# Kernel optimization log

Hardware: AMD Instinct MI355X
Metric: run time of the kernel (lower is better)

The kernel has to match this reference:

```python
import jax, jax.numpy as jnp
import numpy as np

# Dims: B=2, S=2048, D=1024 hidden, E=8 experts, F=2752 ffn (SwiGLU), top-1 gate,
# capacity_factor=1.0 -> capacity C = (B*S)//E = 512. Residual-MoE (moe_use_residual=True).

def setup_inputs() -> dict:
    key = jax.random.key(0)
    ks = jax.random.split(key, 10)
    B, S, D, E, F = 2, 2048, 1024, 8, 2752
    sc = 0.02
    return {
        "hidden_states": jax.random.normal(ks[0], (B, S, D), jnp.float32),
        "wg":  jax.random.normal(ks[1], (D, E), jnp.float32) * sc,   # gate
        "w1":  jax.random.normal(ks[2], (E, D, F), jnp.float32) * sc,  # expert SwiGLU
        "w3":  jax.random.normal(ks[3], (E, D, F), jnp.float32) * sc,
        "w2":  jax.random.normal(ks[4], (E, F, D), jnp.float32) * sc,
        "rw1": jax.random.normal(ks[5], (D, F), jnp.float32) * sc,    # residual MLP (SwiGLU, no bias)
        "rw3": jax.random.normal(ks[6], (D, F), jnp.float32) * sc,
        "rw2": jax.random.normal(ks[7], (F, D), jnp.float32) * sc,
        "cw":  jax.random.normal(ks[8], (D, 2), jnp.float32) * sc,    # coefficient Linear(D, 2)
        "cb":  jnp.zeros((2,), jnp.float32),
    }


def _moe_forward(x, wg, w1, w3, w2):
    """GShard/DeepSpeed-style top-1 gated MoE with capacity + token dropping.
    x: [T, D] flattened tokens. Returns (out [T,D], l_aux scalar, exp_counts [E])."""
    T, D = x.shape
    E = wg.shape[1]
    C = max(4, T // E)  # capacity_factor = 1.0, min_capacity = 4

    logits = x @ wg                                  # [T, E]
    gates = jax.nn.softmax(logits, axis=-1)
    idx = jnp.argmax(gates, axis=-1)                 # top-1 expert per token
    mask1 = jax.nn.one_hot(idx, E, dtype=gates.dtype)  # [T, E]
    exp_counts = jnp.sum(mask1, axis=0).astype(jnp.int32)

    # load-balancing aux loss (DeepSpeed top1gating)
    me = jnp.mean(gates, axis=0)
    ce = jnp.mean(mask1, axis=0)
    l_aux = jnp.sum(me * ce) * E

    # position of each token within its expert's buffer; drop overflow
    locations = jnp.cumsum(mask1, axis=0) - 1.0      # [T, E]
    mask1 = mask1 * (locations < C)
    loc_s = jnp.sum(locations * mask1, axis=1).astype(jnp.int32)  # [T]
    gates1 = jnp.sum(gates * mask1, axis=1)          # [T] gate weight (0 if dropped)

    loc_oh = jax.nn.one_hot(loc_s, C, dtype=gates.dtype)          # [T, C]
    combine = gates1[:, None, None] * mask1[:, :, None] * loc_oh[:, None, :]  # [T, E, C]
    dispatch = (combine > 0).astype(x.dtype)

    xe = jnp.einsum("tec,td->ecd", dispatch, x)      # dispatch to [E, C, D]
    h = jax.nn.silu(jnp.einsum("ecd,edf->ecf", xe, w1)) * jnp.einsum("ecd,edf->ecf", xe, w3)
    ye = jnp.einsum("ecf,efd->ecd", h, w2)           # expert SwiGLU FFN
    out = jnp.einsum("tec,ecd->td", combine, ye)     # weighted combine back to tokens
    return out, l_aux, exp_counts


def reference(hidden_states, wg, w1, w3, w2, rw1, rw3, rw2, cw, cb):
    B, S, D = hidden_states.shape
    x = hidden_states.reshape(-1, D)
    moe_out, l_aux, exp_counts = _moe_forward(x, wg, w1, w3, w2)
    moe_out = moe_out.reshape(B, S, D)

    # residual SwiGLU MLP + softmax-gated combine (Residual-MoE)
    mlp = (jax.nn.silu(hidden_states @ rw1) * (hidden_states @ rw3)) @ rw2
    coef = jax.nn.softmax(hidden_states @ cw + cb, axis=-1)  # [B, S, 2]
    output = moe_out * coef[..., 0:1] + mlp * coef[..., 1:2]
    return output, l_aux, exp_counts
```

## Files before the change

kernel.cpp:

```cpp
#include <hip/hip_runtime.h>
#include <hip/hip_bf16.h>
#include <stdint.h>

#define T_TOK 4096
#define DD 1024
#define EE 8
#define CC 512
#define FF 2752
#define FP 2816

typedef __attribute__((ext_vector_type(8))) short bf16x8;
typedef __attribute__((ext_vector_type(4))) float f32x4;
typedef __attribute__((ext_vector_type(4))) unsigned short us4;
typedef __attribute__((ext_vector_type(8))) unsigned short us8;

__device__ __forceinline__ float bf2f(unsigned short u) {
  union { float f; unsigned int i; } v; v.i = ((unsigned int)u) << 16; return v.f;
}
__device__ __forceinline__ unsigned short f2bf(float f) {
  union { float f; unsigned int i; } v; v.f = f;
  unsigned int r = v.i + 0x7fffu + ((v.i >> 16) & 1u);
  return (unsigned short)(r >> 16);
}

#define GLDS16(g, l) __builtin_amdgcn_global_load_lds( \
    (const __attribute__((address_space(1))) void*)(g), \
    (__attribute__((address_space(3))) void*)(l), 16, 0, 0)

#define STG_CHUNK(l) (((l & 3) ^ ((l >> 3) & 3)) * 8)
#define RD_OFF(fr, fq) ((fr) * 32 + (((fq) ^ (((fr) >> 1) & 3)) * 8))

#define BAR() do { asm volatile("" ::: "memory"); __builtin_amdgcn_s_barrier(); \
                   asm volatile("" ::: "memory"); } while (0)

template<int RT>
__global__ __launch_bounds__(256)
void transpose_k(const float* __restrict__ in, const float* __restrict__ in2,
                 unsigned short* __restrict__ out, unsigned short* __restrict__ out2,
                 int R, int C, long inStride, long outStride) {
  __shared__ unsigned short sm[RT * 64];
  int b = blockIdx.z;
  if (b < EE) { in += (long)b * inStride; out += (long)b * outStride; }
  else { in = in2; out = out2; }
  int cb = blockIdx.x * 64, rb = blockIdx.y * RT;
  int t = threadIdx.x;
  int rr = t >> 4, c4 = (t & 15) * 4;
#pragma unroll
  for (int i = 0; i < RT / 16; ++i) {
    int r = rr + i * 16;
    float4 v = *(const float4*)(in + (long)(rb + r) * C + cb + c4);
    us4 o; o.x = f2bf(v.x); o.y = f2bf(v.y); o.z = f2bf(v.z); o.w = f2bf(v.w);
    *(us4*)&sm[r * 64 + (c4 ^ (((r >> 3) & 7) << 3))] = o;
  }
  __syncthreads();
#pragma unroll
  for (int j = 0; j < (64 * (RT / 8)) / 256; ++j) {
    int idx = t + j * 256;
    int g, c;
    if (RT == 128) { g = idx & 15; c = idx >> 4; }
    else           { g = idx & 7;  c = idx >> 3; }
    int r8 = g * 8;
    us8 o;
#pragma unroll
    for (int k = 0; k < 8; ++k) {
      int r = r8 + k;
      o[k] = sm[r * 64 + (c ^ (((r >> 3) & 7) << 3))];
    }
    *(us8*)(out + (long)(cb + c) * R + rb + r8) = o;
  }
}

__global__ void zero_me_k(float* me) { if (threadIdx.x < EE) me[threadIdx.x] = 0.0f; }

__global__ void gate_k(const float* __restrict__ x, const float* __restrict__ wg,
                       const float* __restrict__ cw, const float* __restrict__ cbv,
                       int* __restrict__ idx, float* __restrict__ gatev,
                       float* __restrict__ coef, float* __restrict__ me_sum) {
  int tid = threadIdx.x, lane = tid & 63, wv = tid >> 6;
  int t = blockIdx.x * 4 + wv;
  const float* xr = x + (long)t * DD;
  float acc[EE] = {0,0,0,0,0,0,0,0};
  float c0 = 0.0f, c1 = 0.0f;
  for (int d = lane; d < DD; d += 64) {
    float xv = xr[d];
#pragma unroll
    for (int e = 0; e < EE; ++e) acc[e] += xv * wg[d * EE + e];
    c0 += xv * cw[d * 2 + 0];
    c1 += xv * cw[d * 2 + 1];
  }
#pragma unroll
  for (int o = 32; o > 0; o >>= 1) {
#pragma unroll
    for (int e = 0; e < EE; ++e) acc[e] += __shfl_xor(acc[e], o);
    c0 += __shfl_xor(c0, o);
    c1 += __shfl_xor(c1, o);
  }
  __shared__ float sme[EE];
  if (tid < EE) sme[tid] = 0.0f;
  __syncthreads();
  if (lane == 0) {
    float m = acc[0]; int am = 0;
#pragma unroll
    for (int e = 1; e < EE; ++e) if (acc[e] > m) { m = acc[e]; am = e; }
    float g[EE]; float s = 0.0f;
#pragma unroll
    for (int e = 0; e < EE; ++e) { g[e] = __expf(acc[e] - m); s += g[e]; }
    float inv = 1.0f / s;
    idx[t] = am;
    gatev[t] = g[am] * inv;
#pragma unroll
    for (int e = 0; e < EE; ++e) atomicAdd(&sme[e], g[e] * inv);
    float l0 = c0 + cbv[0], l1 = c1 + cbv[1];
    float mm = fmaxf(l0, l1);
    float e0 = __expf(l0 - mm), e1 = __expf(l1 - mm);
    float is = 1.0f / (e0 + e1);
    coef[t * 2 + 0] = e0 * is;
    coef[t * 2 + 1] = e1 * is;
  }
  __syncthreads();
  if (tid < EE) atomicAdd(&me_sum[tid], sme[tid]);
}

__global__ void scan_k(const int* __restrict__ idx, const float* __restrict__ me_sum,
                       int* __restrict__ slot, int* __restrict__ tok,
                       float* __restrict__ out_tail) {
  __shared__ int sidx[T_TOK];
  __shared__ int counts[EE];
  int tid = threadIdx.x;
  for (int i = tid; i < T_TOK; i += 512) sidx[i] = idx[i];
  __syncthreads();
  int e = tid >> 6, lane = tid & 63;
  int base = 0;
  for (int it = 0; it < T_TOK / 64; ++it) {
    int t = it * 64 + lane;
    bool f = (sidx[t] == e);
    unsigned long long m = __ballot(f);
    if (f) {
      int loc = base + __popcll(m & ((1ull << lane) - 1ull));
      slot[t] = (loc < CC) ? loc : -1;
      if (loc < CC) tok[e * CC + loc] = t;
    }
    base += __popcll(m);
  }
  if (lane == 0) counts[e] = base;
  __syncthreads();
  int filled = min(counts[e], CC);
  for (int c = filled + lane; c < CC; c += 64) tok[e * CC + c] = -1;
  if (tid == 0) {
    float la = 0.0f;
    for (int i = 0; i < EE; ++i) la += me_sum[i] * (float)counts[i];
    la *= (float)EE / ((float)T_TOK * (float)T_TOK);
    out_tail[0] = la;
    for (int i = 0; i < EE; ++i) out_tail[1 + i] = (float)counts[i];
  }
}

__global__ void gather_k(const float* __restrict__ x, const int* __restrict__ tok,
                         unsigned short* __restrict__ xb, unsigned short* __restrict__ xe) {
  int r = blockIdx.x, tid = threadIdx.x;
  int d = tid * 4;
  if (r < T_TOK) {
    float4 v = *(const float4*)(x + (long)r * DD + d);
    us4 o; o.x = f2bf(v.x); o.y = f2bf(v.y); o.z = f2bf(v.z); o.w = f2bf(v.w);
    *(us4*)(xb + (long)r * DD + d) = o;
  } else {
    int s = r - T_TOK;
    int t = tok[s];
    us4 o = {0, 0, 0, 0};
    if (t >= 0) {
      float4 v = *(const float4*)(x + (long)t * DD + d);
      o.x = f2bf(v.x); o.y = f2bf(v.y); o.z = f2bf(v.z); o.w = f2bf(v.w);
    }
    *(us4*)(xe + (long)s * DD + d) = o;
  }
}

__global__ __launch_bounds__(512, 2)
void gemm1_k(const unsigned short* __restrict__ xcat,
             const unsigned short* __restrict__ w1t, const unsigned short* __restrict__ w3t,
             const unsigned short* __restrict__ rw1t, const unsigned short* __restrict__ rw3t,
             unsigned short* __restrict__ Hcat) {
  int lin = blockIdx.x;
  int work = (lin & 7) * 88 + (lin >> 3);
  int mtile, ntile;
  if (work < 352) {
    int e = work / 44, r = work - e * 44;
    ntile = r >> 1;
    mtile = e * 2 + (r & 1);
  } else {
    int q = work - 352;
    ntile = q >> 4;
    mtile = 16 + (q & 15);
  }
  const unsigned short* A = xcat + (size_t)mtile * 256 * DD;
  const unsigned short *B1, *B3;
  if (mtile < 16) { int e = mtile >> 1; B1 = w1t + (size_t)e * FP * DD; B3 = w3t + (size_t)e * FP * DD; }
  else { B1 = rw1t; B3 = rw3t; }
  unsigned short* H = Hcat + (size_t)mtile * 256 * FF;
  int n0 = ntile * 128;

  __shared__ __align__(16) unsigned short lds[65536];
  char* L = (char*)lds;

  int tid = threadIdx.x, l = tid & 63, w = tid >> 6;
  int wm = w >> 1, wn = w & 1;
  int fr = l & 15, fq = l >> 4;
  int srow = l >> 2, soff = STG_CHUNK(l);
  int rdo = RD_OFF(fr, fq);

  const unsigned short* gA0 = A + (size_t)(w * 16 + srow) * DD + soff;
  const unsigned short* gA1 = A + (size_t)((8 + w) * 16 + srow) * DD + soff;
  const unsigned short* gB1 = B1 + (size_t)(n0 + w * 16 + srow) * DD + soff;
  const unsigned short* gB3 = B3 + (size_t)(n0 + w * 16 + srow) * DD + soff;

#define STG_A(ss, kk, ks) do {                                                    \
    GLDS16(gA0 + (kk) + (ks) * 32, L + (ss) * 32768 + (ks) * 16384 + w * 1024);   \
    GLDS16(gA1 + (kk) + (ks) * 32, L + (ss) * 32768 + (ks) * 16384 + (8 + w) * 1024); } while (0)
#define STG_B(ss, kk, ks) do {                                                    \
    GLDS16(gB1 + (kk) + (ks) * 32, L + 65536 + (ss) * 16384 + (ks) * 8192 + w * 1024); \
    GLDS16(gB3 + (kk) + (ks) * 32, L + 98304 + (ss) * 16384 + (ks) * 8192 + w * 1024); } while (0)

  f32x4 acc1[4][4] = {};
  f32x4 acc3[4][4] = {};
  bf16x8 af[4], b1f[4], b3f[4];

  const int NT = DD / 64;
  STG_A(0, 0, 0); STG_B(0, 0, 0); STG_A(0, 0, 1); STG_B(0, 0, 1);

  for (int t = 0; t < NT; ++t) {
    int s = t & 1, ns = s ^ 1;
    int kk1 = ((t + 1 < NT) ? t + 1 : 0) * 64;

    STG_A(ns, kk1, 0);
    asm volatile("s_waitcnt vmcnt(6)" ::: "memory");
#pragma unroll
    for (int mi = 0; mi < 4; ++mi)
      af[mi] = *(const bf16x8*)(lds + s * 16384 + (wm * 4 + mi) * 512 + rdo);
#pragma unroll
    for (int ni = 0; ni < 4; ++ni)
      b1f[ni] = *(const bf16x8*)(lds + 32768 + s * 8192 + (wn * 4 + ni) * 512 + rdo);
    BAR();
    __builtin_amdgcn_s_setprio(1);
#pragma unroll
    for (int mi = 0; mi < 4; ++mi)
#pragma unroll
      for (int ni = 0; ni < 4; ++ni)
        acc1[mi][ni] = __builtin_amdgcn_mfma_f32_16x16x32_bf16(af[mi], b1f[ni], acc1[mi][ni], 0, 0, 0);
    __builtin_amdgcn_s_setprio(0);
    BAR();

#pragma unroll
    for (int ni = 0; ni < 4; ++ni)
      b3f[ni] = *(const bf16x8*)(lds + 49152 + s * 8192 + (wn * 4 + ni) * 512 + rdo);
    STG_B(ns, kk1, 0);
    BAR();
    __builtin_amdgcn_s_setprio(1);
#pragma unroll
    for (int mi = 0; mi < 4; ++mi)
#pragma unroll
      for (int ni = 0; ni < 4; ++ni)
        acc3[mi][ni] = __builtin_amdgcn_mfma_f32_16x16x32_bf16(af[mi], b3f[ni], acc3[mi][ni], 0, 0, 0);
    __builtin_amdgcn_s_setprio(0);
    BAR();

    STG_A(ns, kk1, 1);
    asm volatile("s_waitcnt vmcnt(6)" ::: "memory");
#pragma unroll
    for (int mi = 0; mi < 4; ++mi)
      af[mi] = *(const bf16x8*)(lds + s * 16384 + 8192 + (wm * 4 + mi) * 512 + rdo);
#pragma unroll
    for (int ni = 0; ni < 4; ++ni)
      b1f[ni] = *(const bf16x8*)(lds + 32768 + s * 8192 + 4096 + (wn * 4 + ni) * 512 + rdo);
    BAR();
    __builtin_amdgcn_s_setprio(1);
#pragma unroll
    for (int mi = 0; mi < 4; ++mi)
#pragma unroll
      for (int ni = 0; ni < 4; ++ni)
        acc1[mi][ni] = __builtin_amdgcn_mfma_f32_16x16x32_bf16(af[mi], b1f[ni], acc1[mi][ni], 0, 0, 0);
    __builtin_amdgcn_s_setprio(0);
    BAR();

#pragma unroll
    for (int ni = 0; ni < 4; ++ni)
      b3f[ni] = *(const bf16x8*)(lds + 49152 + s * 8192 + 4096 + (wn * 4 + ni) * 512 + rdo);
    STG_B(ns, kk1, 1);
    BAR();
    __builtin_amdgcn_s_setprio(1);
#pragma unroll
    for (int mi = 0; mi < 4; ++mi)
#pragma unroll
      for (int ni = 0; ni < 4; ++ni)
        acc3[mi][ni] = __builtin_amdgcn_mfma_f32_16x16x32_bf16(af[mi], b3f[ni], acc3[mi][ni], 0, 0, 0);
    __builtin_amdgcn_s_setprio(0);
    BAR();
  }
#undef STG_A
#undef STG_B

#pragma unroll
  for (int mi = 0; mi < 4; ++mi)
#pragma unroll
    for (int ni = 0; ni < 4; ++ni)
#pragma unroll
      for (int r = 0; r < 4; ++r) {
        int gm = wm * 64 + mi * 16 + fq * 4 + r;
        int gn = n0 + wn * 64 + ni * 16 + fr;
        if (gn < FF) {
          float v1 = acc1[mi][ni][r], v3 = acc3[mi][ni][r];
          float h = v1 / (1.0f + __expf(-v1)) * v3;
          H[(size_t)gm * FF + gn] = f2bf(h);
        }
      }
}

__global__ __launch_bounds__(512, 2)
void gemm2_k(const unsigned short* __restrict__ Hcat,
             const unsigned short* __restrict__ w2t, const unsigned short* __restrict__ rw2t,
             unsigned short* __restrict__ Ycat) {
  int lin = blockIdx.x;
  int work = (lin & 7) * 32 + (lin >> 3);
  int mtile, ntile;
  if (work < 128) {
    int e = work >> 4, r = work & 15;
    ntile = r >> 1;
    mtile = e * 2 + (r & 1);
  } else {
    int q = work - 128;
    ntile = q >> 4;
    mtile = 16 + (q & 15);
  }
  const unsigned short* A = Hcat + (size_t)mtile * 256 * FF;
  const unsigned short* B = (mtile < 16) ? (w2t + (size_t)(mtile >> 1) * DD * FF) : rw2t;
  unsigned short* Y = Ycat + (size_t)mtile * 256 * DD;
  int n0 = ntile * 128;

  __shared__ __align__(16) unsigned short lds[73728];
  char* L = (char*)lds;

  int tid = threadIdx.x, l = tid & 63, w = tid >> 6;
  int wm = w >> 1, wn = w & 1;
  int fr = l & 15, fq = l >> 4;
  int srow = l >> 2, soff = STG_CHUNK(l);
  int rdo = RD_OFF(fr, fq);

  const unsigned short* gA0 = A + (size_t)(w * 16 + srow) * FF + soff;
  const unsigned short* gA1 = A + (size_t)((8 + w) * 16 + srow) * FF + soff;
  const unsigned short* gB  = B + (size_t)(n0 + w * 16 + srow) * FF + soff;

#define STG2(ss, kk, ks) do {                                                        \
    GLDS16(gA0 + (kk) + (ks) * 32, L + (ss) * 32768 + (ks) * 16384 + w * 1024);      \
    GLDS16(gA1 + (kk) + (ks) * 32, L + (ss) * 32768 + (ks) * 16384 + (8 + w) * 1024);\
    GLDS16(gB  + (kk) + (ks) * 32, L + 98304 + (ss) * 16384 + (ks) * 8192 + w * 1024); } while (0)

  f32x4 acc[4][4] = {};
  bf16x8 af[4], bf[4];

  const int NT = FF / 64;
  STG2(0, 0, 0); STG2(0, 0, 1);
  STG2(1, 64, 0); STG2(1, 64, 1);

  for (int t = 0; t < NT; ++t) {
    int st = t % 3;
    int t2 = t + 2; if (t2 >= NT) t2 -= NT;
    int st2 = (st + 2) % 3;
    int kk2 = t2 * 64;

    STG2(st2, kk2, 0);
    asm volatile("s_waitcnt vmcnt(12)" ::: "memory");
#pragma unroll
    for (int mi = 0; mi < 4; ++mi)
      af[mi] = *(const bf16x8*)(lds + st * 16384 + (wm * 4 + mi) * 512 + rdo);
#pragma unroll
    for (int ni = 0; ni < 4; ++ni)
      bf[ni] = *(const bf16x8*)(lds + 49152 + st * 8192 + (wn * 4 + ni) * 512 + rdo);
    BAR();
    __builtin_amdgcn_s_setprio(1);
#pragma unroll
    for (int mi = 0; mi < 4; ++mi)
#pragma unroll
      for (int ni = 0; ni < 4; ++ni)
        acc[mi][ni] = __builtin_amdgcn_mfma_f32_16x16x32_bf16(af[mi], bf[ni], acc[mi][ni], 0, 0, 0);
    __builtin_amdgcn_s_setprio(0);
    BAR();

    STG2(st2, kk2, 1);
    asm volatile("s_waitcnt vmcnt(12)" ::: "memory");
#pragma unroll
    for (int mi = 0; mi < 4; ++mi)
      af[mi] = *(const bf16x8*)(lds + st * 16384 + 8192 + (wm * 4 + mi) * 512 + rdo);
#pragma unroll
    for (int ni = 0; ni < 4; ++ni)
      bf[ni] = *(const bf16x8*)(lds + 49152 + st * 8192 + 4096 + (wn * 4 + ni) * 512 + rdo);
    BAR();
    __builtin_amdgcn_s_setprio(1);
#pragma unroll
    for (int mi = 0; mi < 4; ++mi)
#pragma unroll
      for (int ni = 0; ni < 4; ++ni)
        acc[mi][ni] = __builtin_amdgcn_mfma_f32_16x16x32_bf16(af[mi], bf[ni], acc[mi][ni], 0, 0, 0);
    __builtin_amdgcn_s_setprio(0);
    BAR();
  }
#undef STG2

#pragma unroll
  for (int mi = 0; mi < 4; ++mi)
#pragma unroll
    for (int ni = 0; ni < 4; ++ni)
#pragma unroll
      for (int r = 0; r < 4; ++r) {
        int gm = wm * 64 + mi * 16 + fq * 4 + r;
        int gn = n0 + wn * 64 + ni * 16 + fr;
        Y[(size_t)gm * DD + gn] = f2bf(acc[mi][ni][r]);
      }
}

__global__ void combine_k(const unsigned short* __restrict__ Ye, const unsigned short* __restrict__ Yr,
                          const int* __restrict__ idx, const int* __restrict__ slot,
                          const float* __restrict__ gatev, const float* __restrict__ coef,
                          float* __restrict__ out) {
  int t = blockIdx.x, tid = threadIdx.x;
  int d = tid * 4;
  float c0 = coef[t * 2], c1 = coef[t * 2 + 1];
  int s = slot[t];
  float g = gatev[t] * c0;
  us4 vr = *(const us4*)(Yr + (size_t)t * DD + d);
  float4 o;
  if (s >= 0) {
    us4 ve = *(const us4*)(Ye + ((size_t)idx[t] * CC + s) * DD + d);
    o.x = g * bf2f(ve.x) + c1 * bf2f(vr.x);
    o.y = g * bf2f(ve.y) + c1 * bf2f(vr.y);
    o.z = g * bf2f(ve.z) + c1 * bf2f(vr.z);
    o.w = g * bf2f(ve.w) + c1 * bf2f(vr.w);
  } else {
    o.x = c1 * bf2f(vr.x);
    o.y = c1 * bf2f(vr.y);
    o.z = c1 * bf2f(vr.z);
    o.w = c1 * bf2f(vr.w);
  }
  *(float4*)(out + (size_t)t * DD + d) = o;
}

extern "C" void kernel_launch(void* const* d_in, const int* in_sizes, int n_in,
                              void* d_out, int out_size, void* d_ws, size_t ws_size,
                              hipStream_t stream) {
  const float* x   = (const float*)d_in[0];
  const float* wg  = (const float*)d_in[1];
  const float* w1  = (const float*)d_in[2];
  const float* w3  = (const float*)d_in[3];
  const float* w2  = (const float*)d_in[4];
  const float* rw1 = (const float*)d_in[5];
  const float* rw3 = (const float*)d_in[6];
  const float* rw2 = (const float*)d_in[7];
  const float* cw  = (const float*)d_in[8];
  const float* cbv = (const float*)d_in[9];
  float* out = (float*)d_out;

  char* ws = (char*)d_ws;
  size_t o = 0;
  auto alloc = [&](size_t bytes) -> char* {
    char* p = ws + o; o = (o + bytes + 255) & ~(size_t)255; return p;
  };
  unsigned short* w1t  = (unsigned short*)alloc((size_t)EE * FP * DD * 2);
  unsigned short* w3t  = (unsigned short*)alloc((size_t)EE * FP * DD * 2);
  unsigned short* w2t  = (unsigned short*)alloc((size_t)EE * DD * FF * 2);
  unsigned short* rw1t = (unsigned short*)alloc((size_t)FP * DD * 2);
  unsigned short* rw3t = (unsigned short*)alloc((size_t)FP * DD * 2);
  unsigned short* rw2t = (unsigned short*)alloc((size_t)DD * FF * 2);
  unsigned short* xe   = (unsigned short*)alloc((size_t)T_TOK * DD * 2);
  unsigned short* xb   = (unsigned short*)alloc((size_t)T_TOK * DD * 2);
  unsigned short* He   = (unsigned short*)alloc((size_t)T_TOK * FF * 2);
  unsigned short* Hr   = (unsigned short*)alloc((size_t)T_TOK * FF * 2);
  unsigned short* Ye   = (unsigned short*)alloc((size_t)T_TOK * DD * 2);
  unsigned short* Yr   = (unsigned short*)alloc((size_t)T_TOK * DD * 2);
  int*   idxp  = (int*)alloc(T_TOK * 4);
  float* gatev = (float*)alloc(T_TOK * 4);
  int*   slotp = (int*)alloc(T_TOK * 4);
  int*   tokp  = (int*)alloc(EE * CC * 4);
  float* coefp = (float*)alloc(T_TOK * 2 * 4);
  float* mep   = (float*)alloc(256);
  if (o > ws_size) return;

  transpose_k<128><<<dim3(43, 8, EE + 1), 256, 0, stream>>>(w1, rw1, w1t, rw1t, DD, FF, (long)DD * FF, (long)FP * DD);
  transpose_k<128><<<dim3(43, 8, EE + 1), 256, 0, stream>>>(w3, rw3, w3t, rw3t, DD, FF, (long)DD * FF, (long)FP * DD);
  transpose_k<64><<<dim3(16, 43, EE + 1), 256, 0, stream>>>(w2, rw2, w2t, rw2t, FF, DD, (long)FF * DD, (long)DD * FF);

  zero_me_k<<<1, 64, 0, stream>>>(mep);
  gate_k<<<T_TOK / 4, 256, 0, stream>>>(x, wg, cw, cbv, idxp, gatev, coefp, mep);
  scan_k<<<1, 512, 0, stream>>>(idxp, mep, slotp, tokp, out + (size_t)T_TOK * DD);
  gather_k<<<2 * T_TOK, 256, 0, stream>>>(x, tokp, xb, xe);
  gemm1_k<<<704, 512, 0, stream>>>(xe, w1t, w3t, rw1t, rw3t, He);
  gemm2_k<<<256, 512, 0, stream>>>(He, w2t, rw2t, Ye);
  combine_k<<<T_TOK, 256, 0, stream>>>(Ye, Yr, idxp, slotp, gatev, coefp, out);
}
```

Measured before the change: 302.0 us.

## Deepen GEMM load pipelines with multi-buffer rings of half-width K tiles

Both expert GEMM kernels switch from 64-wide K tiles (double-buffered in the SwiGLU GEMM, triple-buffered in the down-projection) to 32-wide half-tiles held in deeper ring buffers: 4 slots for the gate/up GEMM and 6 slots for the down GEMM. Prefetch runs 3 or 5 half-tiles ahead, with vmcnt waits retuned to match. The aim is to hide more global-to-LDS latency behind MFMA work within the same LDS footprint. The cost is more complex ring indexing and more loop iterations, with their barriers, per K pass.

```diff
diff --git a/kernel.cpp b/kernel.cpp
--- a/kernel.cpp
+++ b/kernel.cpp
@@ -200,7 +200,7 @@
   int n0 = ntile * 128;
 
   __shared__ __align__(16) unsigned short lds[65536];
-  char* L = (char*)lds;
+  char* Lc = (char*)lds;
 
   int tid = threadIdx.x, l = tid & 63, w = tid >> 6;
   int wm = w >> 1, wn = w & 1;
@@ -213,32 +213,37 @@
   const unsigned short* gB1 = B1 + (size_t)(n0 + w * 16 + srow) * DD + soff;
   const unsigned short* gB3 = B3 + (size_t)(n0 + w * 16 + srow) * DD + soff;
 
-#define STG_A(ss, kk, ks) do {                                                    \
-    GLDS16(gA0 + (kk) + (ks) * 32, L + (ss) * 32768 + (ks) * 16384 + w * 1024);   \
-    GLDS16(gA1 + (kk) + (ks) * 32, L + (ss) * 32768 + (ks) * 16384 + (8 + w) * 1024); } while (0)
-#define STG_B(ss, kk, ks) do {                                                    \
-    GLDS16(gB1 + (kk) + (ks) * 32, L + 65536 + (ss) * 16384 + (ks) * 8192 + w * 1024); \
-    GLDS16(gB3 + (kk) + (ks) * 32, L + 98304 + (ss) * 16384 + (ks) * 8192 + w * 1024); } while (0)
+#define STG_A1(bb, kk) do {                                        \
+    GLDS16(gA0 + (kk), Lc + (bb) * 16384 + w * 1024);              \
+    GLDS16(gA1 + (kk), Lc + (bb) * 16384 + (8 + w) * 1024); } while (0)
+#define STG_B1(bb, kk) do {                                        \
+    GLDS16(gB1 + (kk), Lc + 65536 + (bb) * 8192 + w * 1024);       \
+    GLDS16(gB3 + (kk), Lc + 98304 + (bb) * 8192 + w * 1024); } while (0)
 
   f32x4 acc1[4][4] = {};
   f32x4 acc3[4][4] = {};
-  bf16x8 af[4], b1f[4], b3f[4];
-
-  const int NT = DD / 64;
-  STG_A(0, 0, 0); STG_B(0, 0, 0); STG_A(0, 0, 1); STG_B(0, 0, 1);
-
-  for (int t = 0; t < NT; ++t) {
-    int s = t & 1, ns = s ^ 1;
-    int kk1 = ((t + 1 < NT) ? t + 1 : 0) * 64;
-
-    STG_A(ns, kk1, 0);
-    asm volatile("s_waitcnt vmcnt(6)" ::: "memory");
+
+  const int HN = 32;
+#pragma unroll
+  for (int hh = 0; hh < 3; ++hh) { STG_A1(hh, hh * 32); STG_B1(hh, hh * 32); }
+  asm volatile("s_waitcnt vmcnt(8)" ::: "memory");
+  BAR();
+
+#pragma unroll 4
+  for (int h = 0; h < HN; ++h) {
+    int b = h & 3;
+    int hw = h + 3; if (hw >= HN) hw -= HN;
+    int bn = hw & 3;
+    int kk = hw * 32;
+    bf16x8 af[4], b1f[4], b3f[4];
+
 #pragma unroll
     for (int mi = 0; mi < 4; ++mi)
-      af[mi] = *(const bf16x8*)(lds + s * 16384 + (wm * 4 + mi) * 512 + rdo);
+      af[mi] = *(const bf16x8*)(lds + b * 8192 + (wm * 4 + mi) * 512 + rdo);
 #pragma unroll
     for (int ni = 0; ni < 4; ++ni)
-      b1f[ni] = *(const bf16x8*)(lds + 32768 + s * 8192 + (wn * 4 + ni) * 512 + rdo);
+      b1f[ni] = *(const bf16x8*)(lds + 32768 + b * 4096 + (wn * 4 + ni) * 512 + rdo);
+    STG_A1(bn, kk);
     BAR();
     __builtin_amdgcn_s_setprio(1);
 #pragma unroll
@@ -251,8 +256,9 @@
 
 #pragma unroll
     for (int ni = 0; ni < 4; ++ni)
-      b3f[ni] = *(const bf16x8*)(lds + 49152 + s * 8192 + (wn * 4 + ni) * 512 + rdo);
-    STG_B(ns, kk1, 0);
+      b3f[ni] = *(const bf16x8*)(lds + 49152 + b * 4096 + (wn * 4 + ni) * 512 + rdo);
+    STG_B1(bn, kk);
+    asm volatile("s_waitcnt vmcnt(8)" ::: "memory");
     BAR();
     __builtin_amdgcn_s_setprio(1);
 #pragma unroll
@@ -262,41 +268,9 @@
         acc3[mi][ni] = __builtin_amdgcn_mfma_f32_16x16x32_bf16(af[mi], b3f[ni], acc3[mi][ni], 0, 0, 0);
     __builtin_amdgcn_s_setprio(0);
     BAR();
-
-    STG_A(ns, kk1, 1);
-    asm volatile("s_waitcnt vmcnt(6)" ::: "memory");
-#pragma unroll
-    for (int mi = 0; mi < 4; ++mi)
-      af[mi] = *(const bf16x8*)(lds + s * 16384 + 8192 + (wm * 4 + mi) * 512 + rdo);
-#pragma unroll
-    for (int ni = 0; ni < 4; ++ni)
-      b1f[ni] = *(const bf16x8*)(lds + 32768 + s * 8192 + 4096 + (wn * 4 + ni) * 512 + rdo);
-    BAR();
-    __builtin_amdgcn_s_setprio(1);
-#pragma unroll
-    for (int mi = 0; mi < 4; ++mi)
-#pragma unroll
-      for (int ni = 0; ni < 4; ++ni)
-        acc1[mi][ni] = __builtin_amdgcn_mfma_f32_16x16x32_bf16(af[mi], b1f[ni], acc1[mi][ni], 0, 0, 0);
-    __builtin_amdgcn_s_setprio(0);
-    BAR();
-
-#pragma unroll
-    for (int ni = 0; ni < 4; ++ni)
-      b3f[ni] = *(const bf16x8*)(lds + 49152 + s * 8192 + 4096 + (wn * 4 + ni) * 512 + rdo);
-    STG_B(ns, kk1, 1);
-    BAR();
-    __builtin_amdgcn_s_setprio(1);
-#pragma unroll
-    for (int mi = 0; mi < 4; ++mi)
-#pragma unroll
-      for (int ni = 0; ni < 4; ++ni)
-        acc3[mi][ni] = __builtin_amdgcn_mfma_f32_16x16x32_bf16(af[mi], b3f[ni], acc3[mi][ni], 0, 0, 0);
-    __builtin_amdgcn_s_setprio(0);
-    BAR();
-  }
-#undef STG_A
-#undef STG_B
+  }
+#undef STG_A1
+#undef STG_B1
 
 #pragma unroll
   for (int mi = 0; mi < 4; ++mi)
@@ -336,7 +310,7 @@
   int n0 = ntile * 128;
 
   __shared__ __align__(16) unsigned short lds[73728];
-  char* L = (char*)lds;
+  char* Lc = (char*)lds;
 
   int tid = threadIdx.x, l = tid & 63, w = tid >> 6;
   int wm = w >> 1, wn = w & 1;
@@ -348,32 +322,35 @@
   const unsigned short* gA1 = A + (size_t)((8 + w) * 16 + srow) * FF + soff;
   const unsigned short* gB  = B + (size_t)(n0 + w * 16 + srow) * FF + soff;
 
-#define STG2(ss, kk, ks) do {                                                        \
-    GLDS16(gA0 + (kk) + (ks) * 32, L + (ss) * 32768 + (ks) * 16384 + w * 1024);      \
-    GLDS16(gA1 + (kk) + (ks) * 32, L + (ss) * 32768 + (ks) * 16384 + (8 + w) * 1024);\
-    GLDS16(gB  + (kk) + (ks) * 32, L + 98304 + (ss) * 16384 + (ks) * 8192 + w * 1024); } while (0)
+#define STG2(bb, kk) do {                                          \
+    GLDS16(gA0 + (kk), Lc + (bb) * 16384 + w * 1024);              \
+    GLDS16(gA1 + (kk), Lc + (bb) * 16384 + (8 + w) * 1024);        \
+    GLDS16(gB  + (kk), Lc + 98304 + (bb) * 8192 + w * 1024); } while (0)
 
   f32x4 acc[4][4] = {};
-  bf16x8 af[4], bf[4];
-
-  const int NT = FF / 64;
-  STG2(0, 0, 0); STG2(0, 0, 1);
-  STG2(1, 64, 0); STG2(1, 64, 1);
-
-  for (int t = 0; t < NT; ++t) {
-    int st = t % 3;
-    int t2 = t + 2; if (t2 >= NT) t2 -= NT;
-    int st2 = (st + 2) % 3;
-    int kk2 = t2 * 64;
-
-    STG2(st2, kk2, 0);
+
+  const int HN = 86;
+#pragma unroll
+  for (int hh = 0; hh < 5; ++hh) STG2(hh, hh * 32);
+  asm volatile("s_waitcnt vmcnt(12)" ::: "memory");
+  BAR();
+
+  int b = 0;
+#pragma unroll 2
+  for (int h = 0; h < HN; ++h) {
+    int bn = b ? b - 1 : 5;
+    int hw = h + 5; if (hw >= HN) hw -= HN;
+    int kk = hw * 32;
+    bf16x8 af[4], bf[4];
+
+#pragma unroll
+    for (int mi = 0; mi < 4; ++mi)
+      af[mi] = *(const bf16x8*)(lds + b * 8192 + (wm * 4 + mi) * 512 + rdo);
+#pragma unroll
+    for (int ni = 0; ni < 4; ++ni)
+      bf[ni] = *(const bf16x8*)(lds + 49152 + b * 4096 + (wn * 4 + ni) * 512 + rdo);
+    STG2(bn, kk);
     asm volatile("s_waitcnt vmcnt(12)" ::: "memory");
-#pragma unroll
-    for (int mi = 0; mi < 4; ++mi)
-      af[mi] = *(const bf16x8*)(lds + st * 16384 + (wm * 4 + mi) * 512 + rdo);
-#pragma unroll
-    for (int ni = 0; ni < 4; ++ni)
-      bf[ni] = *(const bf16x8*)(lds + 49152 + st * 8192 + (wn * 4 + ni) * 512 + rdo);
     BAR();
     __builtin_amdgcn_s_setprio(1);
 #pragma unroll
@@ -384,23 +361,7 @@
     __builtin_amdgcn_s_setprio(0);
     BAR();
 
-    STG2(st2, kk2, 1);
-    asm volatile("s_waitcnt vmcnt(12)" ::: "memory");
-#pragma unroll
-    for (int mi = 0; mi < 4; ++mi)
-      af[mi] = *(const bf16x8*)(lds + st * 16384 + 8192 + (wm * 4 + mi) * 512 + rdo);
-#pragma unroll
-    for (int ni = 0; ni < 4; ++ni)
-      bf[ni] = *(const bf16x8*)(lds + 49152 + st * 8192 + 4096 + (wn * 4 + ni) * 512 + rdo);
-    BAR();
-    __builtin_amdgcn_s_setprio(1);
-#pragma unroll
-    for (int mi = 0; mi < 4; ++mi)
-#pragma unroll
-      for (int ni = 0; ni < 4; ++ni)
-        acc[mi][ni] = __builtin_amdgcn_mfma_f32_16x16x32_bf16(af[mi], bf[ni], acc[mi][ni], 0, 0, 0);
-    __builtin_amdgcn_s_setprio(0);
-    BAR();
+    ++b; if (b == 6) b = 0;
   }
 #undef STG2
 
```

Result: no change. 303.2 us (+0.4%).
